# Kernel optimization log

Hardware: AMD Instinct MI355X
Metric: run time of the kernel (lower is better)

Reference implementation:

```python
import jax, jax.numpy as jnp
import numpy as np

D_STATE = 16
D_CONV = 4


def rmsnorm(x, w, eps=1e-6):
    # normalize over last (channel) axis
    return x * jax.lax.rsqrt(jnp.mean(x * x, axis=-1, keepdims=True) + eps) * w


def silu(x):
    return x * jax.nn.sigmoid(x)


def mamba(x, in_proj_w, conv1d_w, conv1d_b, x_proj_w, dt_proj_w, dt_proj_b, A_log, D_param, out_proj_w):
    # x: [B, L, C], d_inner == C (expand=1)
    B, L, C = x.shape
    dt_rank = dt_proj_w.shape[1]
    xz = jnp.einsum('blc,ec->ble', x, in_proj_w)  # [B, L, 2C]
    u, z = jnp.split(xz, 2, axis=-1)
    # causal depthwise conv1d over time (pad left d_conv-1)
    uc = jax.lax.conv_general_dilated(
        u.transpose(0, 2, 1), conv1d_w[:, None, :], (1,), [(D_CONV - 1, 0)],
        dimension_numbers=('NCH', 'OIH', 'NCH'), feature_group_count=C)
    u = silu((uc + conv1d_b[None, :, None]).transpose(0, 2, 1))  # [B, L, C]
    x_dbl = jnp.einsum('blc,ec->ble', u, x_proj_w)  # [B, L, dt_rank + 2*N]
    dt, Bm, Cm = jnp.split(x_dbl, [dt_rank, dt_rank + D_STATE], axis=-1)
    delta = jax.nn.softplus(jnp.einsum('blr,dr->bld', dt, dt_proj_w) + dt_proj_b)  # [B, L, C]
    A = -jnp.exp(A_log)  # [C, N]
    deltaA = jnp.exp(delta[..., None] * A)              # [B, L, C, N]
    deltaBu = (delta * u)[..., None] * Bm[:, :, None, :]  # [B, L, C, N]

    def step(h, inp):
        dA, dBu, c = inp
        h = dA * h + dBu
        return h, jnp.einsum('bdn,bn->bd', h, c)

    h0 = jnp.zeros((B, C, D_STATE), x.dtype)
    _, ys = jax.lax.scan(step, h0, (deltaA.transpose(1, 0, 2, 3),
                                    deltaBu.transpose(1, 0, 2, 3),
                                    Cm.transpose(1, 0, 2)))
    y = ys.transpose(1, 0, 2) + u * D_param  # [B, L, C]
    y = y * silu(z)
    return jnp.einsum('bld,od->blo', y, out_proj_w)


def reference(x, norm_w, in_proj_w, conv1d_w, conv1d_b, x_proj_w, dt_proj_w, dt_proj_b,
              A_log, D_param, out_proj_w, scale_mod, dw_w, dw_b, res_scale):
    B, C, H, W = x.shape
    x_cl = x.transpose(0, 2, 3, 1)              # [B, H, W, C]
    xn_cl = rmsnorm(x_cl, norm_w)
    x_norm = xn_cl.transpose(0, 3, 1, 2)        # [B, C, H, W]
    # bidirectional Mamba over flattened spatial sequence
    x_flat = xn_cl.reshape(B, H * W, C)
    mparams = (in_proj_w, conv1d_w, conv1d_b, x_proj_w, dt_proj_w, dt_proj_b, A_log, D_param, out_proj_w)
    fwd = mamba(x_flat, *mparams)
    bwd = jnp.flip(mamba(jnp.flip(x_flat, axis=1), *mparams), axis=1)
    g = (fwd + bwd) * scale_mod
    global_feat = g.reshape(B, H, W, C).transpose(0, 3, 1, 2)
    # local spatial gating: sigmoid(depthwise 3x3 conv) * x_norm
    conv = jax.lax.conv_general_dilated(
        x_norm, dw_w[:, None, :, :], (1, 1), [(1, 1), (1, 1)],
        dimension_numbers=('NCHW', 'OIHW', 'NCHW'), feature_group_count=C)
    local_feat = jax.nn.sigmoid(conv + dw_b[None, :, None, None]) * x_norm
    return x + res_scale * (global_feat + local_feat)


def setup_inputs() -> dict:
    key = jax.random.key(0)
    ks = jax.random.split(key, 10)
    B, C, H, W = 8, 384, 32, 32
    dt_rank = 24  # ceil(384 / 16)
    s = 0.02
    f32 = jnp.float32
    return {
        'x': jax.random.normal(ks[0], (B, C, H, W), f32),
        'norm_w': jnp.ones((C,), f32),
        'in_proj_w': jax.random.normal(ks[1], (2 * C, C), f32) * s,
        'conv1d_w': jax.random.normal(ks[2], (C, D_CONV), f32) * 0.2,
        'conv1d_b': jnp.zeros((C,), f32),
        'x_proj_w': jax.random.normal(ks[3], (dt_rank + 2 * D_STATE, C), f32) * s,
        'dt_proj_w': jax.random.normal(ks[4], (C, dt_rank), f32) * 0.1,
        'dt_proj_b': jax.random.uniform(ks[5], (C,), f32, -4.0, -2.0),
        'A_log': jnp.log(jnp.tile(jnp.arange(1, D_STATE + 1, dtype=f32), (C, 1))),
        'D_param': jnp.ones((C,), f32),
        'out_proj_w': jax.random.normal(ks[6], (C, C), f32) * s,
        'scale_mod': jnp.full((1,), 0.25, f32),
        'dw_w': jax.random.normal(ks[7], (C, 3, 3), f32) * 0.1,
        'dw_b': jnp.zeros((C,), f32),
        'res_scale': jnp.full((1,), 0.5, f32),
    }
```

## Files before the change

kernel.cpp:

```cpp
#include <hip/hip_runtime.h>
#include <hip/hip_bf16.h>


typedef __attribute__((ext_vector_type(8))) short bf16x8;
typedef __attribute__((ext_vector_type(4))) float f32x4;

#define L2E 1.44269504088896340736f

static __device__ __forceinline__ unsigned short f2bf(float f) {
  unsigned int u = __builtin_bit_cast(unsigned int, f);
  u += 0x7fff + ((u >> 16) & 1);
  return (unsigned short)(u >> 16);
}

__global__ __launch_bounds__(256) void prep_k(
    const float* __restrict__ in_w, const float* __restrict__ x_w,
    const float* __restrict__ dt_w, const float* __restrict__ out_w,
    const float* __restrict__ A_log,
    unsigned short* __restrict__ W_in, unsigned short* __restrict__ W_x,
    unsigned short* __restrict__ W_dt, unsigned short* __restrict__ W_out,
    float* __restrict__ A2) {
  int idx = blockIdx.x * 256 + threadIdx.x;
  switch (blockIdx.y) {
    case 0: if (idx < 768 * 384) W_in[idx] = f2bf(in_w[idx]); break;
    case 1: if (idx < 64 * 384) { int n = idx / 384, k = idx - n * 384;
              W_x[idx] = f2bf(n < 56 ? x_w[n * 384 + k] : 0.f); } break;
    case 2: if (idx < 384 * 32) { int n = idx >> 5, k = idx & 31;
              W_dt[idx] = f2bf(k < 24 ? dt_w[n * 24 + k] : 0.f); } break;
    case 3: if (idx < 384 * 384) W_out[idx] = f2bf(out_w[idx]); break;
    case 4: if (idx < 384 * 16) A2[idx] = -expf(A_log[idx]) * L2E; break;
  }
}

__global__ __launch_bounds__(256) void rmsnorm_k(
    const float* __restrict__ x, const float* __restrict__ nw,
    float* __restrict__ xn, unsigned short* __restrict__ xnb) {
  const int b = blockIdx.y;
  const int l0 = blockIdx.x * 32;
  const int tid = threadIdx.x;
  const int ci = tid >> 5, lw = tid & 31;
  __shared__ float part[8][33];
  __shared__ float nf[32];
  __shared__ float t64[64][33];
  float acc = 0.f;
  for (int cc = ci; cc < 384; cc += 8) {
    float v = x[(((size_t)(b * 384 + cc)) << 10) + l0 + lw];
    acc = fmaf(v, v, acc);
  }
  part[ci][lw] = acc;
  __syncthreads();
  if (tid < 32) {
    float s = part[0][tid] + part[1][tid] + part[2][tid] + part[3][tid] +
              part[4][tid] + part[5][tid] + part[6][tid] + part[7][tid];
    nf[tid] = rsqrtf(s * (1.f / 384.f) + 1e-6f);
  }
  __syncthreads();
  const int cr = tid >> 5;
  const int cj = tid & 63, lr = tid >> 6;
  for (int cc = 0; cc < 6; ++cc) {
    #pragma unroll
    for (int k = 0; k < 8; ++k) {
      int cp = cr + k * 8;
      int c = cc * 64 + cp;
      float v = x[(((size_t)(b * 384 + c)) << 10) + l0 + lw];
      t64[cp][lw] = v * nf[lw] * nw[c];
    }
    __syncthreads();
    #pragma unroll
    for (int k2 = 0; k2 < 8; ++k2) {
      int ll = lr + 4 * k2;
      float val = t64[cj][ll];
      size_t a = ((size_t)((b << 10) + l0 + ll)) * 384 + cc * 64 + cj;
      xn[a] = val;
      xnb[a] = f2bf(val);
    }
    __syncthreads();
  }
}

template <int EPI>
__global__ __launch_bounds__(256) void gemm_k(
    const unsigned short* __restrict__ A, const unsigned short* __restrict__ Bw,
    int K, int N,
    float* __restrict__ out0, unsigned short* __restrict__ outb,
    const float* __restrict__ bias, const float* __restrict__ scale) {
  __shared__ unsigned short As[64][40];
  __shared__ unsigned short Bs[64][40];
  const int m0 = blockIdx.x * 64, n0 = blockIdx.y * 64;
  const int tid = threadIdx.x;
  const int lane = tid & 63, wave = tid >> 6;
  const int wm = wave >> 1, wn = wave & 1;
  const int lrow = tid >> 2, lseg = (tid & 3) * 8;
  const int fr = lane & 15, ks = (lane >> 4) * 8;
  f32x4 acc[2][2] = {};
  for (int k0 = 0; k0 < K; k0 += 32) {
    __syncthreads();
    *(bf16x8*)&As[lrow][lseg] = *(const bf16x8*)&A[(size_t)(m0 + lrow) * K + k0 + lseg];
    *(bf16x8*)&Bs[lrow][lseg] = *(const bf16x8*)&Bw[(size_t)(n0 + lrow) * K + k0 + lseg];
    __syncthreads();
    bf16x8 a0 = *(const bf16x8*)&As[wm * 32 + fr][ks];
    bf16x8 a1 = *(const bf16x8*)&As[wm * 32 + 16 + fr][ks];
    bf16x8 b0 = *(const bf16x8*)&Bs[wn * 32 + fr][ks];
    bf16x8 b1 = *(const bf16x8*)&Bs[wn * 32 + 16 + fr][ks];
    acc[0][0] = __builtin_amdgcn_mfma_f32_16x16x32_bf16(a0, b0, acc[0][0], 0, 0, 0);
    acc[0][1] = __builtin_amdgcn_mfma_f32_16x16x32_bf16(a0, b1, acc[0][1], 0, 0, 0);
    acc[1][0] = __builtin_amdgcn_mfma_f32_16x16x32_bf16(a1, b0, acc[1][0], 0, 0, 0);
    acc[1][1] = __builtin_amdgcn_mfma_f32_16x16x32_bf16(a1, b1, acc[1][1], 0, 0, 0);
  }
  #pragma unroll
  for (int mi = 0; mi < 2; ++mi)
    #pragma unroll
    for (int ni = 0; ni < 2; ++ni)
      #pragma unroll
      for (int j = 0; j < 4; ++j) {
        int m = m0 + wm * 32 + mi * 16 + (lane >> 4) * 4 + j;
        int n = n0 + wn * 32 + ni * 16 + (lane & 15);
        float v = acc[mi][ni][j];
        if (EPI == 0) {
          out0[(size_t)m * N + n] = v;
        } else if (EPI == 1) {
          if (n < 24) outb[m * 32 + n] = f2bf(v);
          else if (n < 32) outb[m * 32 + n] = 0;
          if (n >= 24 && n < 56) out0[m * 32 + (n - 24)] = v;
        } else if (EPI == 2) {
          float t = v + bias[n];
          out0[(size_t)m * N + n] = (t > 20.f) ? t : log1pf(expf(t));
        } else {
          out0[(size_t)m * N + n] = v * scale[0];
        }
      }
}

__global__ __launch_bounds__(384) void conv_silu_k(
    const float* __restrict__ xz, const float* __restrict__ cw,
    const float* __restrict__ cb,
    float* __restrict__ u0, float* __restrict__ u1,
    unsigned short* __restrict__ ub0, unsigned short* __restrict__ ub1) {
  const int st = blockIdx.x, b = blockIdx.y, dir = blockIdx.z;
  const int c = threadIdx.x;
  const int s0 = st * 8;
  const float w0 = cw[c * 4 + 0], w1 = cw[c * 4 + 1];
  const float w2 = cw[c * 4 + 2], w3 = cw[c * 4 + 3];
  const float bb = cb[c];
  float* uf = dir ? u1 : u0;
  unsigned short* ub = dir ? ub1 : ub0;
  float xv[11];
  #pragma unroll
  for (int k = 0; k < 11; ++k) {
    int j = s0 - 3 + k;
    float v = 0.f;
    if (j >= 0) {
      int t = dir ? (1023 - j) : j;
      v = xz[(size_t)((b << 10) + t) * 768 + c];
    }
    xv[k] = v;
  }
  #pragma unroll
  for (int s = 0; s < 8; ++s) {
    float a = bb + xv[s] * w0 + xv[s + 1] * w1 + xv[s + 2] * w2 + xv[s + 3] * w3;
    float uv = a * __builtin_amdgcn_rcpf(1.f + __builtin_amdgcn_exp2f(-a * L2E));
    size_t o = (size_t)((b << 10) + s0 + s) * 384 + c;
    uf[o] = uv;
    ub[o] = f2bf(uv);
  }
}

__global__ __launch_bounds__(256) void scan_k(
    const float* __restrict__ d0, const float* __restrict__ d1,
    const float* __restrict__ u0, const float* __restrict__ u1,
    const float* __restrict__ bc0, const float* __restrict__ bc1,
    const float* __restrict__ xz, const float* __restrict__ A2,
    const float* __restrict__ Dp,
    float* __restrict__ S0, float* __restrict__ S1) {
  const int ct = blockIdx.x, b = blockIdx.y, dir = blockIdx.z;
  const float* del = dir ? d1 : d0;
  const float* uu  = dir ? u1 : u0;
  const float* bc  = dir ? bc1 : bc0;
  float* S = dir ? S1 : S0;
  const int tid = threadIdx.x;
  const int lane = tid & 63, wave = tid >> 6;
  const int n = lane & 15, cg = lane >> 4;
  const int cl = wave * 4 + cg;
  const int c = ct * 16 + cl;
  const float a2 = A2[c * 16 + n];
  const float dpc = Dp[c];
  const size_t base = (size_t)b << 10;
  __shared__ __attribute__((aligned(16))) float sd[2][16][20];
  __shared__ __attribute__((aligned(16))) float su[2][16][20];
  __shared__ __attribute__((aligned(16))) float sz[2][16][20];
  __shared__ __attribute__((aligned(16))) float sbc[2][32][20];
  const int li = tid >> 4, lj = tid & 15;
  const int bi = tid >> 5, bj = tid & 31;
  float rd, ru, rz, rb0, rb1;
  auto issue = [&](int s0) {
    size_t row = base + s0 + li;
    rd = del[row * 384 + ct * 16 + lj];
    ru = uu[row * 384 + ct * 16 + lj];
    int t = dir ? (1023 - (s0 + li)) : (s0 + li);
    rz = xz[(base + t) * 768 + 384 + ct * 16 + lj];
    rb0 = bc[(base + s0 + bi) * 32 + bj];
    rb1 = bc[(base + s0 + bi + 8) * 32 + bj];
  };
  auto commit = [&](int buf) {
    sd[buf][lj][li] = rd; su[buf][lj][li] = ru; sz[buf][lj][li] = rz;
    sbc[buf][bj][bi] = rb0; sbc[buf][bj][bi + 8] = rb1;
  };
  issue(0); commit(0);
  float h = 0.f;
  for (int ch = 0; ch < 64; ++ch) {
    const int cur = ch & 1;
    const int s0 = ch * 16;
    if (ch + 1 < 64) issue((ch + 1) * 16);
    __syncthreads();
    f32x4 dv[4], uv4[4], bmv[4], cmv[4];
    #pragma unroll
    for (int r = 0; r < 4; ++r) {
      dv[r]  = *(const f32x4*)&sd[cur][cl][r * 4];
      uv4[r] = *(const f32x4*)&su[cur][cl][r * 4];
      bmv[r] = *(const f32x4*)&sbc[cur][n][r * 4];
      cmv[r] = *(const f32x4*)&sbc[cur][16 + n][r * 4];
    }
    float p[16];
    #pragma unroll
    for (int i = 0; i < 16; ++i) {
      float dd = dv[i >> 2][i & 3];
      float uv = uv4[i >> 2][i & 3];
      float bm = bmv[i >> 2][i & 3];
      float dA = __builtin_amdgcn_exp2f(dd * a2);
      h = fmaf(dA, h, dd * uv * bm);
      p[i] = h * cmv[i >> 2][i & 3];
    }
    float q8[8];
    #pragma unroll
    for (int j = 0; j < 8; ++j) {
      float send = (n & 8) ? p[j] : p[j + 8];
      float recv = __shfl_xor(send, 8);
      float keep = (n & 8) ? p[j + 8] : p[j];
      q8[j] = keep + recv;
    }
    float q4[4];
    #pragma unroll
    for (int j = 0; j < 4; ++j) {
      float send = (n & 4) ? q8[j] : q8[j + 4];
      float recv = __shfl_xor(send, 4);
      float keep = (n & 4) ? q8[j + 4] : q8[j];
      q4[j] = keep + recv;
    }
    float q2[2];
    #pragma unroll
    for (int j = 0; j < 2; ++j) {
      float send = (n & 2) ? q4[j] : q4[j + 2];
      float recv = __shfl_xor(send, 2);
      float keep = (n & 2) ? q4[j + 2] : q4[j];
      q2[j] = keep + recv;
    }
    float send = (n & 1) ? q2[0] : q2[1];
    float recv = __shfl_xor(send, 1);
    float keep = (n & 1) ? q2[1] : q2[0];
    float ysum = keep + recv;
    float uvn = su[cur][cl][n];
    float zz  = sz[cur][cl][n];
    float sig = __builtin_amdgcn_rcpf(1.f + __builtin_amdgcn_exp2f(-zz * L2E));
    float y = (ysum + uvn * dpc) * (zz * sig);
    int s = s0 + n;
    int t = dir ? (1023 - s) : s;
    S[(base + t) * 384 + c] = y;
    if (ch + 1 < 64) commit(cur ^ 1);
  }
}

__global__ __launch_bounds__(256) void ssum_k(
    const float* __restrict__ S0, const float* __restrict__ S1,
    unsigned short* __restrict__ Sb) {
  int i = blockIdx.x * 256 + threadIdx.x;
  float4 a = ((const float4*)S0)[i];
  float4 b = ((const float4*)S1)[i];
  ushort4 r;
  r.x = f2bf(a.x + b.x); r.y = f2bf(a.y + b.y);
  r.z = f2bf(a.z + b.z); r.w = f2bf(a.w + b.w);
  ((ushort4*)Sb)[i] = r;
}

__global__ __launch_bounds__(256) void final_k(
    const float* __restrict__ G, const float* __restrict__ xn,
    const float* __restrict__ x, const float* __restrict__ dww,
    const float* __restrict__ dwb, const float* __restrict__ rs,
    float* __restrict__ out) {
  __shared__ float tile[64][33];
  const int l0 = blockIdx.x * 32, c0 = blockIdx.y * 64, b = blockIdx.z;
  const int tid = threadIdx.x;
  {
    const int cj = tid & 63, li = tid >> 6;
    const int c = c0 + cj;
    float w[9];
    #pragma unroll
    for (int q = 0; q < 9; ++q) w[q] = dww[c * 9 + q];
    const float bb = dwb[c];
    for (int p = 0; p < 8; ++p) {
      int l = l0 + p * 4 + li;
      int hh = l >> 5, ww = l & 31;
      float acc = bb;
      #pragma unroll
      for (int di = -1; di <= 1; ++di) {
        int h2 = hh + di; if (h2 < 0 || h2 > 31) continue;
        #pragma unroll
        for (int dj = -1; dj <= 1; ++dj) {
          int w2 = ww + dj; if (w2 < 0 || w2 > 31) continue;
          acc += xn[(size_t)((b << 10) + h2 * 32 + w2) * 384 + c] * w[(di + 1) * 3 + dj + 1];
        }
      }
      size_t ri = (size_t)((b << 10) + l) * 384 + c;
      float xv = xn[ri];
      float F = G[ri] + xv / (1.f + expf(-acc));
      tile[cj][p * 4 + li] = F;
    }
  }
  __syncthreads();
  {
    const int lw = tid & 31, cr = tid >> 5;
    const float rsv = rs[0];
    for (int p = 0; p < 8; ++p) {
      int c = c0 + p * 8 + cr;
      size_t o = ((size_t)(b * 384 + c) << 10) + l0 + lw;
      out[o] = x[o] + rsv * tile[p * 8 + cr][lw];
    }
  }
}

extern "C" void kernel_launch(void* const* d_in, const int* in_sizes, int n_in,
                              void* d_out, int out_size, void* d_ws, size_t ws_size,
                              hipStream_t stream) {
  const float* x         = (const float*)d_in[0];
  const float* norm_w    = (const float*)d_in[1];
  const float* in_proj_w = (const float*)d_in[2];
  const float* conv1d_w  = (const float*)d_in[3];
  const float* conv1d_b  = (const float*)d_in[4];
  const float* x_proj_w  = (const float*)d_in[5];
  const float* dt_proj_w = (const float*)d_in[6];
  const float* dt_proj_b = (const float*)d_in[7];
  const float* A_log     = (const float*)d_in[8];
  const float* D_param   = (const float*)d_in[9];
  const float* out_proj_w= (const float*)d_in[10];
  const float* scale_mod = (const float*)d_in[11];
  const float* dw_w      = (const float*)d_in[12];
  const float* dw_b      = (const float*)d_in[13];
  const float* res_scale = (const float*)d_in[14];
  float* out = (float*)d_out;

  char* base = (char*)d_ws;
  size_t off = 0;
  auto alloc = [&](size_t bytes) {
    off = (off + 255) & ~(size_t)255;
    void* p = base + off;
    off += bytes;
    return p;
  };
  const size_t F_BLC  = (size_t)8192 * 384 * 4;
  const size_t B_BLC  = (size_t)8192 * 384 * 2;

  float*          xn_f = (float*)alloc(F_BLC);
  unsigned short* xn_b = (unsigned short*)alloc(B_BLC);
  float*          xz   = (float*)alloc((size_t)8192 * 768 * 4);
  float*          u_f0 = (float*)alloc(F_BLC);
  float*          u_f1 = (float*)alloc(F_BLC);
  unsigned short* u_b0 = (unsigned short*)alloc(B_BLC);
  unsigned short* u_b1 = (unsigned short*)alloc(B_BLC);
  unsigned short* dtp0 = (unsigned short*)alloc((size_t)8192 * 32 * 2);
  unsigned short* dtp1 = (unsigned short*)alloc((size_t)8192 * 32 * 2);
  float*          bc0  = (float*)alloc((size_t)8192 * 32 * 4);
  float*          bc1  = (float*)alloc((size_t)8192 * 32 * 4);
  float*          de0  = (float*)alloc(F_BLC);
  float*          de1  = (float*)alloc(F_BLC);
  float*          S0   = (float*)alloc(F_BLC);
  float*          S1   = (float*)alloc(F_BLC);
  unsigned short* W_in = (unsigned short*)alloc((size_t)768 * 384 * 2);
  unsigned short* W_x  = (unsigned short*)alloc((size_t)64 * 384 * 2);
  unsigned short* W_dt = (unsigned short*)alloc((size_t)384 * 32 * 2);
  unsigned short* W_out= (unsigned short*)alloc((size_t)384 * 384 * 2);
  float*          A2   = (float*)alloc((size_t)384 * 16 * 4);
  unsigned short* Ssum = (unsigned short*)de0;
  float*          G    = xz;

  prep_k<<<dim3(1152, 5), 256, 0, stream>>>(in_proj_w, x_proj_w, dt_proj_w,
                                            out_proj_w, A_log,
                                            W_in, W_x, W_dt, W_out, A2);
  rmsnorm_k<<<dim3(32, 8), 256, 0, stream>>>(x, norm_w, xn_f, xn_b);
  gemm_k<0><<<dim3(128, 12), 256, 0, stream>>>(xn_b, W_in, 384, 768, xz,
                                               nullptr, nullptr, nullptr);
  conv_silu_k<<<dim3(128, 8, 2), 384, 0, stream>>>(xz, conv1d_w, conv1d_b,
                                                   u_f0, u_f1, u_b0, u_b1);
  gemm_k<1><<<dim3(128, 1), 256, 0, stream>>>(u_b0, W_x, 384, 64, bc0, dtp0,
                                              nullptr, nullptr);
  gemm_k<1><<<dim3(128, 1), 256, 0, stream>>>(u_b1, W_x, 384, 64, bc1, dtp1,
                                              nullptr, nullptr);
  gemm_k<2><<<dim3(128, 6), 256, 0, stream>>>(dtp0, W_dt, 32, 384, de0,
                                              nullptr, dt_proj_b, nullptr);
  gemm_k<2><<<dim3(128, 6), 256, 0, stream>>>(dtp1, W_dt, 32, 384, de1,
                                              nullptr, dt_proj_b, nullptr);
  scan_k<<<dim3(24, 8, 2), 256, 0, stream>>>(de0, de1, u_f0, u_f1, bc0, bc1,
                                             xz, A2, D_param, S0, S1);
  ssum_k<<<3072, 256, 0, stream>>>(S0, S1, Ssum);
  gemm_k<3><<<dim3(128, 6), 256, 0, stream>>>(Ssum, W_out, 384, 384, G,
                                              nullptr, nullptr, scale_mod);
  final_k<<<dim3(32, 6, 8), 256, 0, stream>>>(G, xn_f, x, dw_w, dw_b,
                                              res_scale, out);
}
```

Measured before the change: 289.4 us.

## Split selective scan into chunked segments and add 128x128 global-to-LDS GEMM

The sequential scan over 1024 steps is divided into 8 segments per sequence. A first pass computes each segment's decay product and end state, a small combine kernel propagates the carried-in states, and a second pass rescans every segment from its carried-in state to produce outputs. This raises grid parallelism from 384 blocks to 3072, at the cost of reading the scan inputs twice. Separately, the in_proj and out_proj GEMMs move to a new 128x128 tile kernel that loads straight from global memory into LDS, and the paired per-direction GEMM launches are merged into single launches using blockIdx.z.

Result: no change. 286.3 us (-1.1%).

```diff
diff --git a/kernel.cpp b/kernel.cpp
--- a/kernel.cpp
+++ b/kernel.cpp
@@ -12,6 +12,11 @@
   u += 0x7fff + ((u >> 16) & 1);
   return (unsigned short)(u >> 16);
 }
+
+#define GLOAD_LDS16(g, l)                                             \
+  __builtin_amdgcn_global_load_lds(                                   \
+      (const __attribute__((address_space(1))) unsigned int*)(g),     \
+      (__attribute__((address_space(3))) unsigned int*)(l), 16, 0, 0)
 
 __global__ __launch_bounds__(256) void prep_k(
     const float* __restrict__ in_w, const float* __restrict__ x_w,
@@ -79,11 +84,70 @@
 }
 
 template <int EPI>
+__global__ __launch_bounds__(256) void gemm128_k(
+    const unsigned short* __restrict__ A, const unsigned short* __restrict__ Bw,
+    int K, int N, float* __restrict__ out0, const float* __restrict__ scale) {
+  __shared__ unsigned short As[128 * 32];
+  __shared__ unsigned short Bs[128 * 32];
+  const int m0 = blockIdx.x * 128, n0 = blockIdx.y * 128;
+  const int tid = threadIdx.x;
+  const int lane = tid & 63, wave = tid >> 6;
+  const int wm = wave >> 1, wn = wave & 1;
+  const int fr = lane & 15, ks = (lane >> 4) * 8;
+  const int row = tid >> 2, colseg = (tid & 3) * 8;
+  const unsigned short* pA0 = A + (size_t)(m0 + row) * K + colseg;
+  const unsigned short* pA1 = A + (size_t)(m0 + 64 + row) * K + colseg;
+  const unsigned short* pB0 = Bw + (size_t)(n0 + row) * K + colseg;
+  const unsigned short* pB1 = Bw + (size_t)(n0 + 64 + row) * K + colseg;
+  unsigned short* lA0 = As + wave * 512;
+  unsigned short* lA1 = As + 2048 + wave * 512;
+  unsigned short* lB0 = Bs + wave * 512;
+  unsigned short* lB1 = Bs + 2048 + wave * 512;
+  f32x4 acc[4][4] = {};
+  for (int k0 = 0; k0 < K; k0 += 32) {
+    __syncthreads();
+    GLOAD_LDS16(pA0, lA0);
+    GLOAD_LDS16(pA1, lA1);
+    GLOAD_LDS16(pB0, lB0);
+    GLOAD_LDS16(pB1, lB1);
+    pA0 += 32; pA1 += 32; pB0 += 32; pB1 += 32;
+    __syncthreads();
+    bf16x8 af[4], bf[4];
+    #pragma unroll
+    for (int mi = 0; mi < 4; ++mi)
+      af[mi] = *(const bf16x8*)&As[(wm * 64 + mi * 16 + fr) * 32 + ks];
+    #pragma unroll
+    for (int ni = 0; ni < 4; ++ni)
+      bf[ni] = *(const bf16x8*)&Bs[(wn * 64 + ni * 16 + fr) * 32 + ks];
+    #pragma unroll
+    for (int mi = 0; mi < 4; ++mi)
+      #pragma unroll
+      for (int ni = 0; ni < 4; ++ni)
+        acc[mi][ni] = __builtin_amdgcn_mfma_f32_16x16x32_bf16(af[mi], bf[ni], acc[mi][ni], 0, 0, 0);
+  }
+  const float sc = (EPI == 3) ? scale[0] : 1.f;
+  #pragma unroll
+  for (int mi = 0; mi < 4; ++mi)
+    #pragma unroll
+    for (int ni = 0; ni < 4; ++ni)
+      #pragma unroll
+      for (int j = 0; j < 4; ++j) {
+        int m = m0 + wm * 64 + mi * 16 + (lane >> 4) * 4 + j;
+        int n = n0 + wn * 64 + ni * 16 + fr;
+        out0[(size_t)m * N + n] = acc[mi][ni][j] * sc;
+      }
+}
+
+template <int EPI>
 __global__ __launch_bounds__(256) void gemm_k(
-    const unsigned short* __restrict__ A, const unsigned short* __restrict__ Bw,
-    int K, int N,
-    float* __restrict__ out0, unsigned short* __restrict__ outb,
-    const float* __restrict__ bias, const float* __restrict__ scale) {
+    const unsigned short* __restrict__ A0u, const unsigned short* __restrict__ A1u,
+    const unsigned short* __restrict__ Bw, int K, int N,
+    float* __restrict__ o0a, float* __restrict__ o0b,
+    unsigned short* __restrict__ oba, unsigned short* __restrict__ obb,
+    const float* __restrict__ bias) {
+  const unsigned short* A = blockIdx.z ? A1u : A0u;
+  float* out0 = blockIdx.z ? o0b : o0a;
+  unsigned short* outb = blockIdx.z ? obb : oba;
   __shared__ unsigned short As[64][40];
   __shared__ unsigned short Bs[64][40];
   const int m0 = blockIdx.x * 64, n0 = blockIdx.y * 64;
@@ -116,17 +180,13 @@
         int m = m0 + wm * 32 + mi * 16 + (lane >> 4) * 4 + j;
         int n = n0 + wn * 32 + ni * 16 + (lane & 15);
         float v = acc[mi][ni][j];
-        if (EPI == 0) {
-          out0[(size_t)m * N + n] = v;
-        } else if (EPI == 1) {
+        if (EPI == 1) {
           if (n < 24) outb[m * 32 + n] = f2bf(v);
           else if (n < 32) outb[m * 32 + n] = 0;
           if (n >= 24 && n < 56) out0[m * 32 + (n - 24)] = v;
-        } else if (EPI == 2) {
+        } else {
           float t = v + bias[n];
           out0[(size_t)m * N + n] = (t > 20.f) ? t : log1pf(expf(t));
-        } else {
-          out0[(size_t)m * N + n] = v * scale[0];
         }
       }
 }
@@ -165,14 +225,89 @@
   }
 }
 
-__global__ __launch_bounds__(256) void scan_k(
+__global__ __launch_bounds__(256) void scan1_k(
+    const float* __restrict__ d0, const float* __restrict__ d1,
+    const float* __restrict__ u0, const float* __restrict__ u1,
+    const float* __restrict__ bc0, const float* __restrict__ bc1,
+    const float* __restrict__ A2,
+    float* __restrict__ Pseg, float* __restrict__ Hseg) {
+  const int ct = blockIdx.x, b = blockIdx.y;
+  const int dir = blockIdx.z >> 3, seg = blockIdx.z & 7;
+  const float* del = dir ? d1 : d0;
+  const float* uu  = dir ? u1 : u0;
+  const float* bc  = dir ? bc1 : bc0;
+  const int tid = threadIdx.x;
+  const int lane = tid & 63, wave = tid >> 6;
+  const int n = lane & 15, cg = lane >> 4;
+  const int cl = wave * 4 + cg;
+  const int c = ct * 16 + cl;
+  const float a2 = A2[c * 16 + n];
+  const size_t base = ((size_t)b << 10) + seg * 128;
+  __shared__ __attribute__((aligned(16))) float sd[2][16][20];
+  __shared__ __attribute__((aligned(16))) float su[2][16][20];
+  __shared__ __attribute__((aligned(16))) float sB[2][16][20];
+  const int li = tid >> 4, lj = tid & 15;
+  float rd, ru, rb;
+  auto issue = [&](int s0) {
+    size_t rowi = base + s0 + li;
+    rd = del[rowi * 384 + ct * 16 + lj];
+    ru = uu [rowi * 384 + ct * 16 + lj];
+    rb = bc [rowi * 32 + lj];
+  };
+  auto commit = [&](int buf) {
+    sd[buf][lj][li] = rd; su[buf][lj][li] = ru; sB[buf][lj][li] = rb;
+  };
+  issue(0); commit(0);
+  float h = 0.f, P = 1.f;
+  for (int ch = 0; ch < 8; ++ch) {
+    const int cur = ch & 1;
+    if (ch + 1 < 8) issue((ch + 1) * 16);
+    __syncthreads();
+    f32x4 dv[4], uv4[4], bmv[4];
+    #pragma unroll
+    for (int r = 0; r < 4; ++r) {
+      dv[r]  = *(const f32x4*)&sd[cur][cl][r * 4];
+      uv4[r] = *(const f32x4*)&su[cur][cl][r * 4];
+      bmv[r] = *(const f32x4*)&sB[cur][n][r * 4];
+    }
+    #pragma unroll
+    for (int i = 0; i < 16; ++i) {
+      float dd = dv[i >> 2][i & 3];
+      float uv = uv4[i >> 2][i & 3];
+      float bm = bmv[i >> 2][i & 3];
+      float dA = __builtin_amdgcn_exp2f(dd * a2);
+      h = fmaf(dA, h, dd * uv * bm);
+      P *= dA;
+    }
+    if (ch + 1 < 8) { __syncthreads(); commit(cur ^ 1); }
+  }
+  size_t o = (size_t)((dir * 8 + b) * 8 + seg) * 6144 + c * 16 + n;
+  Pseg[o] = P; Hseg[o] = h;
+}
+
+__global__ __launch_bounds__(256) void scomb_k(
+    const float* __restrict__ Pseg, const float* __restrict__ Hseg,
+    float* __restrict__ Hin) {
+  const int db = blockIdx.y;
+  const int r = blockIdx.x * 256 + threadIdx.x;
+  float h = 0.f;
+  #pragma unroll
+  for (int s = 0; s < 8; ++s) {
+    size_t o = (size_t)(db * 8 + s) * 6144 + r;
+    Hin[o] = h;
+    h = Pseg[o] * h + Hseg[o];
+  }
+}
+
+__global__ __launch_bounds__(256) void scan2_k(
     const float* __restrict__ d0, const float* __restrict__ d1,
     const float* __restrict__ u0, const float* __restrict__ u1,
     const float* __restrict__ bc0, const float* __restrict__ bc1,
     const float* __restrict__ xz, const float* __restrict__ A2,
-    const float* __restrict__ Dp,
+    const float* __restrict__ Dp, const float* __restrict__ Hin,
     float* __restrict__ S0, float* __restrict__ S1) {
-  const int ct = blockIdx.x, b = blockIdx.y, dir = blockIdx.z;
+  const int ct = blockIdx.x, b = blockIdx.y;
+  const int dir = blockIdx.z >> 3, seg = blockIdx.z & 7;
   const float* del = dir ? d1 : d0;
   const float* uu  = dir ? u1 : u0;
   const float* bc  = dir ? bc1 : bc0;
@@ -185,6 +320,7 @@
   const float a2 = A2[c * 16 + n];
   const float dpc = Dp[c];
   const size_t base = (size_t)b << 10;
+  const int segoff = seg * 128;
   __shared__ __attribute__((aligned(16))) float sd[2][16][20];
   __shared__ __attribute__((aligned(16))) float su[2][16][20];
   __shared__ __attribute__((aligned(16))) float sz[2][16][20];
@@ -193,24 +329,23 @@
   const int bi = tid >> 5, bj = tid & 31;
   float rd, ru, rz, rb0, rb1;
   auto issue = [&](int s0) {
-    size_t row = base + s0 + li;
-    rd = del[row * 384 + ct * 16 + lj];
-    ru = uu[row * 384 + ct * 16 + lj];
-    int t = dir ? (1023 - (s0 + li)) : (s0 + li);
+    size_t rowi = base + segoff + s0 + li;
+    rd = del[rowi * 384 + ct * 16 + lj];
+    ru = uu [rowi * 384 + ct * 16 + lj];
+    int t = dir ? (1023 - (segoff + s0 + li)) : (segoff + s0 + li);
     rz = xz[(base + t) * 768 + 384 + ct * 16 + lj];
-    rb0 = bc[(base + s0 + bi) * 32 + bj];
-    rb1 = bc[(base + s0 + bi + 8) * 32 + bj];
+    rb0 = bc[(base + segoff + s0 + bi) * 32 + bj];
+    rb1 = bc[(base + segoff + s0 + bi + 8) * 32 + bj];
   };
   auto commit = [&](int buf) {
     sd[buf][lj][li] = rd; su[buf][lj][li] = ru; sz[buf][lj][li] = rz;
     sbc[buf][bj][bi] = rb0; sbc[buf][bj][bi + 8] = rb1;
   };
   issue(0); commit(0);
-  float h = 0.f;
-  for (int ch = 0; ch < 64; ++ch) {
+  float h = Hin[(size_t)((dir * 8 + b) * 8 + seg) * 6144 + c * 16 + n];
+  for (int ch = 0; ch < 8; ++ch) {
     const int cur = ch & 1;
-    const int s0 = ch * 16;
-    if (ch + 1 < 64) issue((ch + 1) * 16);
+    if (ch + 1 < 8) issue((ch + 1) * 16);
     __syncthreads();
     f32x4 dv[4], uv4[4], bmv[4], cmv[4];
     #pragma unroll
@@ -262,10 +397,10 @@
     float zz  = sz[cur][cl][n];
     float sig = __builtin_amdgcn_rcpf(1.f + __builtin_amdgcn_exp2f(-zz * L2E));
     float y = (ysum + uvn * dpc) * (zz * sig);
-    int s = s0 + n;
+    int s = segoff + ch * 16 + n;
     int t = dir ? (1023 - s) : s;
     S[(base + t) * 384 + c] = y;
-    if (ch + 1 < 64) commit(cur ^ 1);
+    if (ch + 1 < 8) { __syncthreads(); commit(cur ^ 1); }
   }
 }
 
@@ -373,6 +508,9 @@
   float*          de1  = (float*)alloc(F_BLC);
   float*          S0   = (float*)alloc(F_BLC);
   float*          S1   = (float*)alloc(F_BLC);
+  float*          Pseg = (float*)alloc((size_t)786432 * 4);
+  float*          Hseg = (float*)alloc((size_t)786432 * 4);
+  float*          Hin  = (float*)alloc((size_t)786432 * 4);
   unsigned short* W_in = (unsigned short*)alloc((size_t)768 * 384 * 2);
   unsigned short* W_x  = (unsigned short*)alloc((size_t)64 * 384 * 2);
   unsigned short* W_dt = (unsigned short*)alloc((size_t)384 * 32 * 2);
@@ -385,23 +523,22 @@
                                             out_proj_w, A_log,
                                             W_in, W_x, W_dt, W_out, A2);
   rmsnorm_k<<<dim3(32, 8), 256, 0, stream>>>(x, norm_w, xn_f, xn_b);
-  gemm_k<0><<<dim3(128, 12), 256, 0, stream>>>(xn_b, W_in, 384, 768, xz,
-                                               nullptr, nullptr, nullptr);
+  gemm128_k<0><<<dim3(64, 6), 256, 0, stream>>>(xn_b, W_in, 384, 768, xz, nullptr);
   conv_silu_k<<<dim3(128, 8, 2), 384, 0, stream>>>(xz, conv1d_w, conv1d_b,
                                                    u_f0, u_f1, u_b0, u_b1);
-  gemm_k<1><<<dim3(128, 1), 256, 0, stream>>>(u_b0, W_x, 384, 64, bc0, dtp0,
-                                              nullptr, nullptr);
-  gemm_k<1><<<dim3(128, 1), 256, 0, stream>>>(u_b1, W_x, 384, 64, bc1, dtp1,
-                                              nullptr, nullptr);
-  gemm_k<2><<<dim3(128, 6), 256, 0, stream>>>(dtp0, W_dt, 32, 384, de0,
-                                              nullptr, dt_proj_b, nullptr);
-  gemm_k<2><<<dim3(128, 6), 256, 0, stream>>>(dtp1, W_dt, 32, 384, de1,
-                                              nullptr, dt_proj_b, nullptr);
-  scan_k<<<dim3(24, 8, 2), 256, 0, stream>>>(de0, de1, u_f0, u_f1, bc0, bc1,
-                                             xz, A2, D_param, S0, S1);
+  gemm_k<1><<<dim3(128, 1, 2), 256, 0, stream>>>(u_b0, u_b1, W_x, 384, 64,
+                                                 bc0, bc1, dtp0, dtp1, nullptr);
+  gemm_k<2><<<dim3(128, 6, 2), 256, 0, stream>>>(dtp0, dtp1, W_dt, 32, 384,
+                                                 de0, de1, nullptr, nullptr,
+                                                 dt_proj_b);
+  scan1_k<<<dim3(24, 8, 16), 256, 0, stream>>>(de0, de1, u_f0, u_f1, bc0, bc1,
+                                               A2, Pseg, Hseg);
+  scomb_k<<<dim3(24, 16), 256, 0, stream>>>(Pseg, Hseg, Hin);
+  scan2_k<<<dim3(24, 8, 16), 256, 0, stream>>>(de0, de1, u_f0, u_f1, bc0, bc1,
+                                               xz, A2, D_param, Hin, S0, S1);
   ssum_k<<<3072, 256, 0, stream>>>(S0, S1, Ssum);
-  gemm_k<3><<<dim3(128, 6), 256, 0, stream>>>(Ssum, W_out, 384, 384, G,
-                                              nullptr, nullptr, scale_mod);
+  gemm128_k<3><<<dim3(64, 3), 256, 0, stream>>>(Ssum, W_out, 384, 384, G,
+                                                scale_mod);
   final_k<<<dim3(32, 6, 8), 256, 0, stream>>>(G, xn_f, x, dw_w, dw_b,
                                               res_scale, out);
 }
```

## Chunk the selective scan into parallel segments and store intermediates in bf16

Applied to the files above, without the earlier changes.

Replaces the sequential 1024-step scan, which launched only 384 blocks, with a three-phase segmented scan over 16 segments. The phases compute each segment's decay product and end state, combine carries across segments, then rerun each segment from its carried-in state. The change also folds the norm weight into W_in and applies the per-token rsqrt in the in_proj epilogue. It stores xz, u, delta and the scan outputs in bf16 instead of fp32 and merges the paired per-direction GEMM launches via blockIdx.z. This gives far more parallelism and less memory traffic, at the cost of rerunning the recurrence and lower intermediate precision.

After: 263.6 us. 1.1x faster.

```diff
diff --git a/kernel.cpp b/kernel.cpp
--- a/kernel.cpp
+++ b/kernel.cpp
@@ -3,6 +3,7 @@
 
 
 typedef __attribute__((ext_vector_type(8))) short bf16x8;
+typedef __attribute__((ext_vector_type(8))) unsigned short u16x8;
 typedef __attribute__((ext_vector_type(4))) float f32x4;
 
 #define L2E 1.44269504088896340736f
@@ -12,17 +13,21 @@
   u += 0x7fff + ((u >> 16) & 1);
   return (unsigned short)(u >> 16);
 }
+static __device__ __forceinline__ float bf2f(unsigned short u) {
+  unsigned int v = (unsigned int)u << 16;
+  return __builtin_bit_cast(float, v);
+}
 
 __global__ __launch_bounds__(256) void prep_k(
     const float* __restrict__ in_w, const float* __restrict__ x_w,
     const float* __restrict__ dt_w, const float* __restrict__ out_w,
-    const float* __restrict__ A_log,
+    const float* __restrict__ A_log, const float* __restrict__ nw,
     unsigned short* __restrict__ W_in, unsigned short* __restrict__ W_x,
     unsigned short* __restrict__ W_dt, unsigned short* __restrict__ W_out,
     float* __restrict__ A2) {
   int idx = blockIdx.x * 256 + threadIdx.x;
   switch (blockIdx.y) {
-    case 0: if (idx < 768 * 384) W_in[idx] = f2bf(in_w[idx]); break;
+    case 0: if (idx < 768 * 384) W_in[idx] = f2bf(in_w[idx] * nw[idx % 384]); break;
     case 1: if (idx < 64 * 384) { int n = idx / 384, k = idx - n * 384;
               W_x[idx] = f2bf(n < 56 ? x_w[n * 384 + k] : 0.f); } break;
     case 2: if (idx < 384 * 32) { int n = idx >> 5, k = idx & 31;
@@ -32,58 +37,53 @@
   }
 }
 
-__global__ __launch_bounds__(256) void rmsnorm_k(
-    const float* __restrict__ x, const float* __restrict__ nw,
-    float* __restrict__ xn, unsigned short* __restrict__ xnb) {
+__global__ __launch_bounds__(256) void transpose_k(
+    const float* __restrict__ x, unsigned short* __restrict__ xb,
+    float* __restrict__ nf) {
   const int b = blockIdx.y;
   const int l0 = blockIdx.x * 32;
   const int tid = threadIdx.x;
-  const int ci = tid >> 5, lw = tid & 31;
+  const int cr = tid >> 5, lw = tid & 31;
+  const int cj = tid & 63, lr = tid >> 6;
+  __shared__ float t64[64][33];
   __shared__ float part[8][33];
-  __shared__ float nf[32];
-  __shared__ float t64[64][33];
   float acc = 0.f;
-  for (int cc = ci; cc < 384; cc += 8) {
-    float v = x[(((size_t)(b * 384 + cc)) << 10) + l0 + lw];
-    acc = fmaf(v, v, acc);
-  }
-  part[ci][lw] = acc;
+  for (int cc = 0; cc < 6; ++cc) {
+    #pragma unroll
+    for (int k = 0; k < 8; ++k) {
+      int cp = k * 8 + cr;
+      int c = cc * 64 + cp;
+      float v = x[(((size_t)(b * 384 + c)) << 10) + l0 + lw];
+      t64[cp][lw] = v;
+      acc = fmaf(v, v, acc);
+    }
+    __syncthreads();
+    #pragma unroll
+    for (int k2 = 0; k2 < 8; ++k2) {
+      int ll = lr + 4 * k2;
+      xb[((size_t)((b << 10) + l0 + ll)) * 384 + cc * 64 + cj] = f2bf(t64[cj][ll]);
+    }
+    __syncthreads();
+  }
+  part[cr][lw] = acc;
   __syncthreads();
   if (tid < 32) {
     float s = part[0][tid] + part[1][tid] + part[2][tid] + part[3][tid] +
               part[4][tid] + part[5][tid] + part[6][tid] + part[7][tid];
-    nf[tid] = rsqrtf(s * (1.f / 384.f) + 1e-6f);
-  }
-  __syncthreads();
-  const int cr = tid >> 5;
-  const int cj = tid & 63, lr = tid >> 6;
-  for (int cc = 0; cc < 6; ++cc) {
-    #pragma unroll
-    for (int k = 0; k < 8; ++k) {
-      int cp = cr + k * 8;
-      int c = cc * 64 + cp;
-      float v = x[(((size_t)(b * 384 + c)) << 10) + l0 + lw];
-      t64[cp][lw] = v * nf[lw] * nw[c];
-    }
-    __syncthreads();
-    #pragma unroll
-    for (int k2 = 0; k2 < 8; ++k2) {
-      int ll = lr + 4 * k2;
-      float val = t64[cj][ll];
-      size_t a = ((size_t)((b << 10) + l0 + ll)) * 384 + cc * 64 + cj;
-      xn[a] = val;
-      xnb[a] = f2bf(val);
-    }
-    __syncthreads();
+    nf[(b << 10) + l0 + tid] = rsqrtf(s * (1.f / 384.f) + 1e-6f);
   }
 }
 
 template <int EPI>
 __global__ __launch_bounds__(256) void gemm_k(
-    const unsigned short* __restrict__ A, const unsigned short* __restrict__ Bw,
-    int K, int N,
-    float* __restrict__ out0, unsigned short* __restrict__ outb,
-    const float* __restrict__ bias, const float* __restrict__ scale) {
+    const unsigned short* __restrict__ A0u, const unsigned short* __restrict__ A1u,
+    const unsigned short* __restrict__ Bw, int K, int N,
+    float* __restrict__ of0, float* __restrict__ of1,
+    unsigned short* __restrict__ ob0, unsigned short* __restrict__ ob1,
+    const float* __restrict__ aux) {
+  const unsigned short* A = blockIdx.z ? A1u : A0u;
+  float* outf = blockIdx.z ? of1 : of0;
+  unsigned short* outb = blockIdx.z ? ob1 : ob0;
   __shared__ unsigned short As[64][40];
   __shared__ unsigned short Bs[64][40];
   const int m0 = blockIdx.x * 64, n0 = blockIdx.y * 64;
@@ -117,24 +117,24 @@
         int n = n0 + wn * 32 + ni * 16 + (lane & 15);
         float v = acc[mi][ni][j];
         if (EPI == 0) {
-          out0[(size_t)m * N + n] = v;
+          outb[(size_t)m * N + n] = f2bf(v * aux[m]);
         } else if (EPI == 1) {
           if (n < 24) outb[m * 32 + n] = f2bf(v);
           else if (n < 32) outb[m * 32 + n] = 0;
-          if (n >= 24 && n < 56) out0[m * 32 + (n - 24)] = v;
+          if (n >= 24 && n < 56) outf[m * 32 + (n - 24)] = v;
         } else if (EPI == 2) {
-          float t = v + bias[n];
-          out0[(size_t)m * N + n] = (t > 20.f) ? t : log1pf(expf(t));
+          float t = v + aux[n];
+          float sp = (t > 20.f) ? t : log1pf(expf(t));
+          outb[(size_t)m * N + n] = f2bf(sp);
         } else {
-          out0[(size_t)m * N + n] = v * scale[0];
+          outf[(size_t)m * N + n] = v * aux[0];
         }
       }
 }
 
 __global__ __launch_bounds__(384) void conv_silu_k(
-    const float* __restrict__ xz, const float* __restrict__ cw,
+    const unsigned short* __restrict__ xz, const float* __restrict__ cw,
     const float* __restrict__ cb,
-    float* __restrict__ u0, float* __restrict__ u1,
     unsigned short* __restrict__ ub0, unsigned short* __restrict__ ub1) {
   const int st = blockIdx.x, b = blockIdx.y, dir = blockIdx.z;
   const int c = threadIdx.x;
@@ -142,7 +142,6 @@
   const float w0 = cw[c * 4 + 0], w1 = cw[c * 4 + 1];
   const float w2 = cw[c * 4 + 2], w3 = cw[c * 4 + 3];
   const float bb = cb[c];
-  float* uf = dir ? u1 : u0;
   unsigned short* ub = dir ? ub1 : ub0;
   float xv[11];
   #pragma unroll
@@ -151,7 +150,7 @@
     float v = 0.f;
     if (j >= 0) {
       int t = dir ? (1023 - j) : j;
-      v = xz[(size_t)((b << 10) + t) * 768 + c];
+      v = bf2f(xz[(size_t)((b << 10) + t) * 768 + c]);
     }
     xv[k] = v;
   }
@@ -159,24 +158,95 @@
   for (int s = 0; s < 8; ++s) {
     float a = bb + xv[s] * w0 + xv[s + 1] * w1 + xv[s + 2] * w2 + xv[s + 3] * w3;
     float uv = a * __builtin_amdgcn_rcpf(1.f + __builtin_amdgcn_exp2f(-a * L2E));
-    size_t o = (size_t)((b << 10) + s0 + s) * 384 + c;
-    uf[o] = uv;
-    ub[o] = f2bf(uv);
-  }
-}
-
-__global__ __launch_bounds__(256) void scan_k(
-    const float* __restrict__ d0, const float* __restrict__ d1,
-    const float* __restrict__ u0, const float* __restrict__ u1,
+    ub[(size_t)((b << 10) + s0 + s) * 384 + c] = f2bf(uv);
+  }
+}
+
+__global__ __launch_bounds__(256) void scan1_k(
+    const unsigned short* __restrict__ de0, const unsigned short* __restrict__ de1,
+    const unsigned short* __restrict__ ub0, const unsigned short* __restrict__ ub1,
     const float* __restrict__ bc0, const float* __restrict__ bc1,
-    const float* __restrict__ xz, const float* __restrict__ A2,
-    const float* __restrict__ Dp,
-    float* __restrict__ S0, float* __restrict__ S1) {
-  const int ct = blockIdx.x, b = blockIdx.y, dir = blockIdx.z;
-  const float* del = dir ? d1 : d0;
-  const float* uu  = dir ? u1 : u0;
+    const float* __restrict__ A2,
+    float* __restrict__ Pseg, float* __restrict__ Hseg) {
+  const int ct = blockIdx.x, b = blockIdx.y;
+  const int dir = blockIdx.z >> 4, seg = blockIdx.z & 15;
+  const unsigned short* del = dir ? de1 : de0;
+  const unsigned short* uu  = dir ? ub1 : ub0;
   const float* bc  = dir ? bc1 : bc0;
-  float* S = dir ? S1 : S0;
+  const int tid = threadIdx.x;
+  const int lane = tid & 63, wave = tid >> 6;
+  const int n = lane & 15, cg = lane >> 4;
+  const int cl = wave * 4 + cg;
+  const int c = ct * 16 + cl;
+  const float a2 = A2[c * 16 + n];
+  const size_t base = ((size_t)b << 10) + seg * 64;
+  __shared__ __attribute__((aligned(16))) float sd[2][16][20];
+  __shared__ __attribute__((aligned(16))) float sdu[2][16][20];
+  __shared__ __attribute__((aligned(16))) float sB[2][16][20];
+  const int li = tid >> 4, lj = tid & 15;
+  unsigned short rd, ru; float rb;
+  auto issue = [&](int s0) {
+    size_t rowi = base + s0 + li;
+    rd = del[rowi * 384 + ct * 16 + lj];
+    ru = uu [rowi * 384 + ct * 16 + lj];
+    rb = bc [rowi * 32 + lj];
+  };
+  auto commit = [&](int buf) {
+    float dd = bf2f(rd), uv = bf2f(ru);
+    sd[buf][lj][li] = dd; sdu[buf][lj][li] = dd * uv; sB[buf][lj][li] = rb;
+  };
+  issue(0); commit(0);
+  float h = 0.f, P = 1.f;
+  for (int ch = 0; ch < 4; ++ch) {
+    const int cur = ch & 1;
+    if (ch + 1 < 4) issue((ch + 1) * 16);
+    __syncthreads();
+    f32x4 dv[4], duv[4], bmv[4];
+    #pragma unroll
+    for (int r = 0; r < 4; ++r) {
+      dv[r]  = *(const f32x4*)&sd[cur][cl][r * 4];
+      duv[r] = *(const f32x4*)&sdu[cur][cl][r * 4];
+      bmv[r] = *(const f32x4*)&sB[cur][n][r * 4];
+    }
+    #pragma unroll
+    for (int i = 0; i < 16; ++i) {
+      float dA = __builtin_amdgcn_exp2f(dv[i >> 2][i & 3] * a2);
+      h = fmaf(dA, h, duv[i >> 2][i & 3] * bmv[i >> 2][i & 3]);
+      P *= dA;
+    }
+    if (ch + 1 < 4) { __syncthreads(); commit(cur ^ 1); }
+  }
+  size_t o = (size_t)((dir * 8 + b) * 16 + seg) * 6144 + c * 16 + n;
+  Pseg[o] = P; Hseg[o] = h;
+}
+
+__global__ __launch_bounds__(256) void scomb_k(
+    const float* __restrict__ Pseg, const float* __restrict__ Hseg,
+    float* __restrict__ Hin) {
+  const int db = blockIdx.y;
+  const int r = blockIdx.x * 256 + threadIdx.x;
+  float h = 0.f;
+  #pragma unroll
+  for (int s = 0; s < 16; ++s) {
+    size_t o = (size_t)(db * 16 + s) * 6144 + r;
+    Hin[o] = h;
+    h = Pseg[o] * h + Hseg[o];
+  }
+}
+
+__global__ __launch_bounds__(256) void scan2_k(
+    const unsigned short* __restrict__ de0, const unsigned short* __restrict__ de1,
+    const unsigned short* __restrict__ ub0, const unsigned short* __restrict__ ub1,
+    const float* __restrict__ bc0, const float* __restrict__ bc1,
+    const unsigned short* __restrict__ xz, const float* __restrict__ A2,
+    const float* __restrict__ Dp, const float* __restrict__ Hin,
+    unsigned short* __restrict__ Sb0, unsigned short* __restrict__ Sb1) {
+  const int ct = blockIdx.x, b = blockIdx.y;
+  const int dir = blockIdx.z >> 4, seg = blockIdx.z & 15;
+  const unsigned short* del = dir ? de1 : de0;
+  const unsigned short* uu  = dir ? ub1 : ub0;
+  const float* bc  = dir ? bc1 : bc0;
+  unsigned short* S = dir ? Sb1 : Sb0;
   const int tid = threadIdx.x;
   const int lane = tid & 63, wave = tid >> 6;
   const int n = lane & 15, cg = lane >> 4;
@@ -185,49 +255,49 @@
   const float a2 = A2[c * 16 + n];
   const float dpc = Dp[c];
   const size_t base = (size_t)b << 10;
+  const int segoff = seg * 64;
   __shared__ __attribute__((aligned(16))) float sd[2][16][20];
+  __shared__ __attribute__((aligned(16))) float sdu[2][16][20];
   __shared__ __attribute__((aligned(16))) float su[2][16][20];
   __shared__ __attribute__((aligned(16))) float sz[2][16][20];
   __shared__ __attribute__((aligned(16))) float sbc[2][32][20];
   const int li = tid >> 4, lj = tid & 15;
   const int bi = tid >> 5, bj = tid & 31;
-  float rd, ru, rz, rb0, rb1;
+  unsigned short rd, ru, rz; float rb0, rb1;
   auto issue = [&](int s0) {
-    size_t row = base + s0 + li;
-    rd = del[row * 384 + ct * 16 + lj];
-    ru = uu[row * 384 + ct * 16 + lj];
-    int t = dir ? (1023 - (s0 + li)) : (s0 + li);
+    size_t rowi = base + segoff + s0 + li;
+    rd = del[rowi * 384 + ct * 16 + lj];
+    ru = uu [rowi * 384 + ct * 16 + lj];
+    int t = dir ? (1023 - (segoff + s0 + li)) : (segoff + s0 + li);
     rz = xz[(base + t) * 768 + 384 + ct * 16 + lj];
-    rb0 = bc[(base + s0 + bi) * 32 + bj];
-    rb1 = bc[(base + s0 + bi + 8) * 32 + bj];
+    rb0 = bc[(base + segoff + s0 + bi) * 32 + bj];
+    rb1 = bc[(base + segoff + s0 + bi + 8) * 32 + bj];
   };
   auto commit = [&](int buf) {
-    sd[buf][lj][li] = rd; su[buf][lj][li] = ru; sz[buf][lj][li] = rz;
+    float dd = bf2f(rd), uv = bf2f(ru);
+    sd[buf][lj][li] = dd; sdu[buf][lj][li] = dd * uv;
+    su[buf][lj][li] = uv; sz[buf][lj][li] = bf2f(rz);
     sbc[buf][bj][bi] = rb0; sbc[buf][bj][bi + 8] = rb1;
   };
   issue(0); commit(0);
-  float h = 0.f;
-  for (int ch = 0; ch < 64; ++ch) {
+  float h = Hin[(size_t)((dir * 8 + b) * 16 + seg) * 6144 + c * 16 + n];
+  for (int ch = 0; ch < 4; ++ch) {
     const int cur = ch & 1;
-    const int s0 = ch * 16;
-    if (ch + 1 < 64) issue((ch + 1) * 16);
-    __syncthreads();
-    f32x4 dv[4], uv4[4], bmv[4], cmv[4];
+    if (ch + 1 < 4) issue((ch + 1) * 16);
+    __syncthreads();
+    f32x4 dv[4], duv[4], bmv[4], cmv[4];
     #pragma unroll
     for (int r = 0; r < 4; ++r) {
       dv[r]  = *(const f32x4*)&sd[cur][cl][r * 4];
-      uv4[r] = *(const f32x4*)&su[cur][cl][r * 4];
+      duv[r] = *(const f32x4*)&sdu[cur][cl][r * 4];
       bmv[r] = *(const f32x4*)&sbc[cur][n][r * 4];
       cmv[r] = *(const f32x4*)&sbc[cur][16 + n][r * 4];
     }
     float p[16];
     #pragma unroll
     for (int i = 0; i < 16; ++i) {
-      float dd = dv[i >> 2][i & 3];
-      float uv = uv4[i >> 2][i & 3];
-      float bm = bmv[i >> 2][i & 3];
-      float dA = __builtin_amdgcn_exp2f(dd * a2);
-      h = fmaf(dA, h, dd * uv * bm);
+      float dA = __builtin_amdgcn_exp2f(dv[i >> 2][i & 3] * a2);
+      h = fmaf(dA, h, duv[i >> 2][i & 3] * bmv[i >> 2][i & 3]);
       p[i] = h * cmv[i >> 2][i & 3];
     }
     float q8[8];
@@ -262,27 +332,28 @@
     float zz  = sz[cur][cl][n];
     float sig = __builtin_amdgcn_rcpf(1.f + __builtin_amdgcn_exp2f(-zz * L2E));
     float y = (ysum + uvn * dpc) * (zz * sig);
-    int s = s0 + n;
+    int s = segoff + ch * 16 + n;
     int t = dir ? (1023 - s) : s;
-    S[(base + t) * 384 + c] = y;
-    if (ch + 1 < 64) commit(cur ^ 1);
+    S[(base + t) * 384 + c] = f2bf(y);
+    if (ch + 1 < 4) { __syncthreads(); commit(cur ^ 1); }
   }
 }
 
 __global__ __launch_bounds__(256) void ssum_k(
-    const float* __restrict__ S0, const float* __restrict__ S1,
+    const unsigned short* __restrict__ S0, const unsigned short* __restrict__ S1,
     unsigned short* __restrict__ Sb) {
   int i = blockIdx.x * 256 + threadIdx.x;
-  float4 a = ((const float4*)S0)[i];
-  float4 b = ((const float4*)S1)[i];
-  ushort4 r;
-  r.x = f2bf(a.x + b.x); r.y = f2bf(a.y + b.y);
-  r.z = f2bf(a.z + b.z); r.w = f2bf(a.w + b.w);
-  ((ushort4*)Sb)[i] = r;
+  u16x8 a = ((const u16x8*)S0)[i];
+  u16x8 b = ((const u16x8*)S1)[i];
+  u16x8 r;
+  #pragma unroll
+  for (int j = 0; j < 8; ++j) r[j] = f2bf(bf2f(a[j]) + bf2f(b[j]));
+  ((u16x8*)Sb)[i] = r;
 }
 
 __global__ __launch_bounds__(256) void final_k(
-    const float* __restrict__ G, const float* __restrict__ xn,
+    const float* __restrict__ G, const unsigned short* __restrict__ xb,
+    const float* __restrict__ nf, const float* __restrict__ nw,
     const float* __restrict__ x, const float* __restrict__ dww,
     const float* __restrict__ dwb, const float* __restrict__ rs,
     float* __restrict__ out) {
@@ -296,6 +367,7 @@
     #pragma unroll
     for (int q = 0; q < 9; ++q) w[q] = dww[c * 9 + q];
     const float bb = dwb[c];
+    const float nwc = nw[c];
     for (int p = 0; p < 8; ++p) {
       int l = l0 + p * 4 + li;
       int hh = l >> 5, ww = l & 31;
@@ -306,11 +378,14 @@
         #pragma unroll
         for (int dj = -1; dj <= 1; ++dj) {
           int w2 = ww + dj; if (w2 < 0 || w2 > 31) continue;
-          acc += xn[(size_t)((b << 10) + h2 * 32 + w2) * 384 + c] * w[(di + 1) * 3 + dj + 1];
+          int lp = h2 * 32 + w2;
+          float xnv = bf2f(xb[(size_t)((b << 10) + lp) * 384 + c]) *
+                      nf[(b << 10) + lp] * nwc;
+          acc += xnv * w[(di + 1) * 3 + dj + 1];
         }
       }
       size_t ri = (size_t)((b << 10) + l) * 384 + c;
-      float xv = xn[ri];
+      float xv = bf2f(xb[ri]) * nf[(b << 10) + l] * nwc;
       float F = G[ri] + xv / (1.f + expf(-acc));
       tile[cj][p * 4 + li] = F;
     }
@@ -355,53 +430,53 @@
     off += bytes;
     return p;
   };
-  const size_t F_BLC  = (size_t)8192 * 384 * 4;
-  const size_t B_BLC  = (size_t)8192 * 384 * 2;
-
-  float*          xn_f = (float*)alloc(F_BLC);
-  unsigned short* xn_b = (unsigned short*)alloc(B_BLC);
-  float*          xz   = (float*)alloc((size_t)8192 * 768 * 4);
-  float*          u_f0 = (float*)alloc(F_BLC);
-  float*          u_f1 = (float*)alloc(F_BLC);
+  const size_t B_BLC = (size_t)8192 * 384 * 2;
+
+  unsigned short* xb   = (unsigned short*)alloc(B_BLC);
+  float*          nf   = (float*)alloc((size_t)8192 * 4);
+  unsigned short* xz   = (unsigned short*)alloc((size_t)8192 * 768 * 2);
   unsigned short* u_b0 = (unsigned short*)alloc(B_BLC);
   unsigned short* u_b1 = (unsigned short*)alloc(B_BLC);
   unsigned short* dtp0 = (unsigned short*)alloc((size_t)8192 * 32 * 2);
   unsigned short* dtp1 = (unsigned short*)alloc((size_t)8192 * 32 * 2);
   float*          bc0  = (float*)alloc((size_t)8192 * 32 * 4);
   float*          bc1  = (float*)alloc((size_t)8192 * 32 * 4);
-  float*          de0  = (float*)alloc(F_BLC);
-  float*          de1  = (float*)alloc(F_BLC);
-  float*          S0   = (float*)alloc(F_BLC);
-  float*          S1   = (float*)alloc(F_BLC);
+  unsigned short* de0  = (unsigned short*)alloc(B_BLC);
+  unsigned short* de1  = (unsigned short*)alloc(B_BLC);
+  unsigned short* Sb0  = (unsigned short*)alloc(B_BLC);
+  unsigned short* Sb1  = (unsigned short*)alloc(B_BLC);
+  float*          Pseg = (float*)alloc((size_t)1572864 * 4);
+  float*          Hseg = (float*)alloc((size_t)1572864 * 4);
+  float*          Hin  = (float*)alloc((size_t)1572864 * 4);
   unsigned short* W_in = (unsigned short*)alloc((size_t)768 * 384 * 2);
   unsigned short* W_x  = (unsigned short*)alloc((size_t)64 * 384 * 2);
   unsigned short* W_dt = (unsigned short*)alloc((size_t)384 * 32 * 2);
   unsigned short* W_out= (unsigned short*)alloc((size_t)384 * 384 * 2);
   float*          A2   = (float*)alloc((size_t)384 * 16 * 4);
-  unsigned short* Ssum = (unsigned short*)de0;
-  float*          G    = xz;
+  float*          G    = (float*)alloc((size_t)8192 * 384 * 4);
+  unsigned short* Ssum = de0;
 
   prep_k<<<dim3(1152, 5), 256, 0, stream>>>(in_proj_w, x_proj_w, dt_proj_w,
-                                            out_proj_w, A_log,
+                                            out_proj_w, A_log, norm_w,
                                             W_in, W_x, W_dt, W_out, A2);
-  rmsnorm_k<<<dim3(32, 8), 256, 0, stream>>>(x, norm_w, xn_f, xn_b);
-  gemm_k<0><<<dim3(128, 12), 256, 0, stream>>>(xn_b, W_in, 384, 768, xz,
-                                               nullptr, nullptr, nullptr);
+  transpose_k<<<dim3(32, 8), 256, 0, stream>>>(x, xb, nf);
+  gemm_k<0><<<dim3(128, 12), 256, 0, stream>>>(xb, xb, W_in, 384, 768,
+                                               nullptr, nullptr, xz, xz, nf);
   conv_silu_k<<<dim3(128, 8, 2), 384, 0, stream>>>(xz, conv1d_w, conv1d_b,
-                                                   u_f0, u_f1, u_b0, u_b1);
-  gemm_k<1><<<dim3(128, 1), 256, 0, stream>>>(u_b0, W_x, 384, 64, bc0, dtp0,
-                                              nullptr, nullptr);
-  gemm_k<1><<<dim3(128, 1), 256, 0, stream>>>(u_b1, W_x, 384, 64, bc1, dtp1,
-                                              nullptr, nullptr);
-  gemm_k<2><<<dim3(128, 6), 256, 0, stream>>>(dtp0, W_dt, 32, 384, de0,
-                                              nullptr, dt_proj_b, nullptr);
-  gemm_k<2><<<dim3(128, 6), 256, 0, stream>>>(dtp1, W_dt, 32, 384, de1,
-                                              nullptr, dt_proj_b, nullptr);
-  scan_k<<<dim3(24, 8, 2), 256, 0, stream>>>(de0, de1, u_f0, u_f1, bc0, bc1,
-                                             xz, A2, D_param, S0, S1);
-  ssum_k<<<3072, 256, 0, stream>>>(S0, S1, Ssum);
-  gemm_k<3><<<dim3(128, 6), 256, 0, stream>>>(Ssum, W_out, 384, 384, G,
-                                              nullptr, nullptr, scale_mod);
-  final_k<<<dim3(32, 6, 8), 256, 0, stream>>>(G, xn_f, x, dw_w, dw_b,
+                                                   u_b0, u_b1);
+  gemm_k<1><<<dim3(128, 1, 2), 256, 0, stream>>>(u_b0, u_b1, W_x, 384, 64,
+                                                 bc0, bc1, dtp0, dtp1, nullptr);
+  gemm_k<2><<<dim3(128, 6, 2), 256, 0, stream>>>(dtp0, dtp1, W_dt, 32, 384,
+                                                 nullptr, nullptr, de0, de1,
+                                                 dt_proj_b);
+  scan1_k<<<dim3(24, 8, 32), 256, 0, stream>>>(de0, de1, u_b0, u_b1, bc0, bc1,
+                                               A2, Pseg, Hseg);
+  scomb_k<<<dim3(24, 16), 256, 0, stream>>>(Pseg, Hseg, Hin);
+  scan2_k<<<dim3(24, 8, 32), 256, 0, stream>>>(de0, de1, u_b0, u_b1, bc0, bc1,
+                                               xz, A2, D_param, Hin, Sb0, Sb1);
+  ssum_k<<<1536, 256, 0, stream>>>(Sb0, Sb1, Ssum);
+  gemm_k<3><<<dim3(128, 6), 256, 0, stream>>>(Ssum, Ssum, W_out, 384, 384,
+                                              G, G, nullptr, nullptr, scale_mod);
+  final_k<<<dim3(32, 6, 8), 256, 0, stream>>>(G, xb, nf, norm_w, x, dw_w, dw_b,
                                               res_scale, out);
 }
```
